# Kernel tuning notes

Measured on AMD Instinct MI355X. Metric: run time of the kernel, lower is better.

Reference implementation:

```python
import jax, jax.numpy as jnp
import numpy as np

C = 256          # C_in == C_out
G = C // 4       # groups = C_in/4 -> 4 channels per group
K = 3
STRIDE = 1
PAD = 2
DIL = 2
EPS = 1e-5

@jax.custom_vjp
def binarize(x):
    # 1-bit sign binarization with straight-through estimator (STE)
    return jnp.sign(x)

def _bin_fwd(x):
    return jnp.sign(x), x

def _bin_bwd(x, g):
    # STE with hardtanh clip: pass grad where |x| <= 1
    return (g * (jnp.abs(x) <= 1.0).astype(g.dtype),)

binarize.defvjp(_bin_fwd, _bin_bwd)

def setup_inputs() -> dict:
    key = jax.random.key(0)
    k1, k2, k3, k4, k5, k6 = jax.random.split(key, 6)
    x = jax.random.normal(k1, (64, C, 32, 32), jnp.float32)
    # grouped conv weight: [C_out, C_in/groups, K, K] = [256, 4, 3, 3]
    weight = jax.random.normal(k2, (C, C // G, K, K), jnp.float32) * 0.1
    gamma = 1.0 + 0.1 * jax.random.normal(k3, (C,), jnp.float32)
    beta = 0.1 * jax.random.normal(k4, (C,), jnp.float32)
    running_mean = 0.1 * jax.random.normal(k5, (C,), jnp.float32)
    running_var = jax.random.uniform(k6, (C,), jnp.float32, 0.5, 1.5)
    return {"x": x, "weight": weight, "gamma": gamma, "beta": beta,
            "running_mean": running_mean, "running_var": running_var}

def reference(x, weight, gamma, beta, running_mean, running_var):
    # BatchNorm2d (inference form with running stats)
    inv = gamma * jax.lax.rsqrt(running_var + EPS)            # [C]
    h = x * inv[None, :, None, None] + (beta - running_mean * inv)[None, :, None, None]
    # binarize activations and weights (1w1a)
    a = binarize(h)
    w = binarize(weight)
    # grouped dilated conv, stride 1, pad 2, dilation 2 -> same HxW
    out = jax.lax.conv_general_dilated(
        a, w,
        window_strides=(STRIDE, STRIDE),
        padding=[(PAD, PAD), (PAD, PAD)],
        rhs_dilation=(DIL, DIL),
        dimension_numbers=("NCHW", "OIHW", "NCHW"),
        feature_group_count=G)
    # channel shuffle: [N,C,H,W] -> [N,g,C/g,H,W] -> [N,C/g,g,H,W] -> [N,C,H,W]
    N, Cc, H, W = out.shape
    out = out.reshape(N, G, Cc // G, H, W).transpose(0, 2, 1, 3, 4).reshape(N, Cc, H, W)
    # identity shortcut (stride == 1)
    return out + x
```

## Files before the change

### kernel.cpp

```cpp
#include <hip/hip_runtime.h>

#ifndef __has_builtin
#define __has_builtin(x) 0
#endif

#if __has_builtin(__builtin_amdgcn_sdot4)
#define DOT4(a, b, c) __builtin_amdgcn_sdot4((a), (b), (c), false)
#else
__device__ __forceinline__ int dot4_sw(int a, int b, int c) {
#pragma unroll
    for (int k = 0; k < 4; ++k)
        c += (int)(signed char)((a >> (8 * k)) & 0xff) *
             (int)(signed char)((b >> (8 * k)) & 0xff);
    return c;
}
#define DOT4(a, b, c) dot4_sw((a), (b), (c))
#endif

constexpr int CH   = 256;
constexpr int NPIX = 1024;
constexpr float BN_EPS = 1e-5f;

__device__ __forceinline__ float rfl_f(float v) {
    return __int_as_float(__builtin_amdgcn_readfirstlane(__float_as_int(v)));
}

__global__ __launch_bounds__(256) void bconv(const float* __restrict__ x,
                                             const float* __restrict__ wgt,
                                             const float* __restrict__ gamma,
                                             const float* __restrict__ beta,
                                             const float* __restrict__ rmean,
                                             const float* __restrict__ rvar,
                                             float* __restrict__ out) {
    __shared__ int   wq_lds[36];
    __shared__ float bn_lds[8];

    const int tid  = threadIdx.x;
    const int n    = blockIdx.x >> 6;
    const int g    = blockIdx.x & 63;
    const int pix0 = tid * 4;
    const int row  = pix0 >> 5;
    const int col0 = pix0 & 31;
    const float* xn = x + n * CH * NPIX;
    float* on = out + n * CH * NPIX;

    float4 xv[3][4];
#pragma unroll
    for (int kh = 0; kh < 3; ++kh) {
        const int rs  = row + 2 * kh - 2;
        const int rsc = min(max(rs, 0), 31);
        const float* rp = xn + g * 4 * NPIX + rsc * 32 + col0;
#pragma unroll
        for (int ci = 0; ci < 4; ++ci)
            xv[kh][ci] = *(const float4*)(rp + ci * NPIX);
    }
    float4 sc[4];
#pragma unroll
    for (int c2 = 0; c2 < 4; ++c2)
        sc[c2] = *(const float4*)(xn + (c2 * 64 + g) * NPIX + pix0);

    if (tid < 144) {
        const int c2 = tid / 36, r = tid % 36, ci = r / 9, tap = r % 9;
        float w = wgt[g * 144 + tid];
        int s = (w > 0.f) ? 1 : ((w < 0.f) ? -1 : 0);
        ((char*)wq_lds)[(c2 * 9 + tap) * 4 + ci] = (char)s;
    } else if (tid < 148) {
        const int ci = tid - 144, c = g * 4 + ci;
        float r  = __fdiv_rn(1.0f, __fsqrt_rn(__fadd_rn(rvar[c], BN_EPS)));
        float iv = __fmul_rn(gamma[c], r);
        bn_lds[ci]     = iv;
        bn_lds[4 + ci] = __fsub_rn(beta[c], __fmul_rn(rmean[c], iv));
    }
    __syncthreads();

    int wq[4][9];
#pragma unroll
    for (int c2 = 0; c2 < 4; ++c2)
#pragma unroll
        for (int t = 0; t < 9; ++t)
            wq[c2][t] = __builtin_amdgcn_readfirstlane(wq_lds[c2 * 9 + t]);
    float inv[4], bias[4];
#pragma unroll
    for (int ci = 0; ci < 4; ++ci) {
        inv[ci]  = rfl_f(bn_lds[ci]);
        bias[ci] = rfl_f(bn_lds[4 + ci]);
    }

    int pkc[3][4];
#pragma unroll
    for (int kh = 0; kh < 3; ++kh) {
        const bool ok = (unsigned)(row + 2 * kh - 2) < 32u;
#pragma unroll
        for (int p = 0; p < 4; ++p) {
            int v = 0;
#pragma unroll
            for (int ci = 0; ci < 4; ++ci) {
                float h = __fadd_rn(__fmul_rn(((const float*)&xv[kh][ci])[p], inv[ci]), bias[ci]);
                int s = (h > 0.f) ? 1 : ((h < 0.f) ? -1 : 0);
                v |= (s & 0xff) << (8 * ci);
            }
            pkc[kh][p] = ok ? v : 0;
        }
    }

    const bool le = (col0 == 0), re = (col0 == 28);
    int a[3][8];
#pragma unroll
    for (int kh = 0; kh < 3; ++kh) {
        int l2 = __shfl_up(pkc[kh][2], 1);
        int l3 = __shfl_up(pkc[kh][3], 1);
        int r0 = __shfl_down(pkc[kh][0], 1);
        int r1 = __shfl_down(pkc[kh][1], 1);
        a[kh][0] = le ? 0 : l2;
        a[kh][1] = le ? 0 : l3;
        a[kh][2] = pkc[kh][0]; a[kh][3] = pkc[kh][1];
        a[kh][4] = pkc[kh][2]; a[kh][5] = pkc[kh][3];
        a[kh][6] = re ? 0 : r0;
        a[kh][7] = re ? 0 : r1;
    }

#pragma unroll
    for (int c2 = 0; c2 < 4; ++c2) {
        float4 o;
#pragma unroll
        for (int p = 0; p < 4; ++p) {
            int acc = 0;
#pragma unroll
            for (int kh = 0; kh < 3; ++kh)
#pragma unroll
                for (int kw = 0; kw < 3; ++kw)
                    acc = DOT4(a[kh][p + 2 * kw], wq[c2][kh * 3 + kw], acc);
            ((float*)&o)[p] = __fadd_rn((float)acc, ((const float*)&sc[c2])[p]);
        }
        *(float4*)(on + (c2 * 64 + g) * NPIX + pix0) = o;
    }
}

extern "C" void kernel_launch(void* const* d_in, const int* in_sizes, int n_in,
                              void* d_out, int out_size, void* d_ws, size_t ws_size,
                              hipStream_t stream) {
    const float* x     = (const float*)d_in[0];
    const float* wgt   = (const float*)d_in[1];
    const float* gamma = (const float*)d_in[2];
    const float* beta  = (const float*)d_in[3];
    const float* rmean = (const float*)d_in[4];
    const float* rvar  = (const float*)d_in[5];
    float* out = (float*)d_out;

    const int N = in_sizes[0] / (CH * NPIX);
    bconv<<<N * 64, 256, 0, stream>>>(x, wgt, gamma, beta, rmean, rvar, out);
}
```

Measured before the change: 34.59 us.

## Process two batch images per block and prefetch second image's input

Each block now handles two consecutive batch images for the same channel group, halving the grid size and amortizing the weight binarization and BN-parameter setup across both. The second image's input rows are loaded while the first image's packed activations are computed and stored, overlapping global loads with compute. A launch-bounds occupancy hint of four blocks is added. This raises register pressure and assumes an even batch size.

```diff
diff --git a/kernel.cpp b/kernel.cpp
--- a/kernel.cpp
+++ b/kernel.cpp
@@ -25,39 +25,46 @@
     return __int_as_float(__builtin_amdgcn_readfirstlane(__float_as_int(v)));
 }
 
-__global__ __launch_bounds__(256) void bconv(const float* __restrict__ x,
-                                             const float* __restrict__ wgt,
-                                             const float* __restrict__ gamma,
-                                             const float* __restrict__ beta,
-                                             const float* __restrict__ rmean,
-                                             const float* __restrict__ rvar,
-                                             float* __restrict__ out) {
+__global__ __launch_bounds__(256, 4)
+void bconv(const float* __restrict__ x,
+           const float* __restrict__ wgt,
+           const float* __restrict__ gamma,
+           const float* __restrict__ beta,
+           const float* __restrict__ rmean,
+           const float* __restrict__ rvar,
+           float* __restrict__ out) {
     __shared__ int   wq_lds[36];
     __shared__ float bn_lds[8];
 
     const int tid  = threadIdx.x;
-    const int n    = blockIdx.x >> 6;
+    const int n0   = (blockIdx.x >> 6) * 2;
     const int g    = blockIdx.x & 63;
     const int pix0 = tid * 4;
     const int row  = pix0 >> 5;
     const int col0 = pix0 & 31;
-    const float* xn = x + n * CH * NPIX;
-    float* on = out + n * CH * NPIX;
+    const float* xnA = x + n0 * CH * NPIX;
+    const float* xnB = xnA + CH * NPIX;
+    float* onA = out + n0 * CH * NPIX;
+    float* onB = onA + CH * NPIX;
 
     float4 xv[3][4];
+    auto load_xv = [&](const float* xn) {
 #pragma unroll
-    for (int kh = 0; kh < 3; ++kh) {
-        const int rs  = row + 2 * kh - 2;
-        const int rsc = min(max(rs, 0), 31);
-        const float* rp = xn + g * 4 * NPIX + rsc * 32 + col0;
+        for (int kh = 0; kh < 3; ++kh) {
+            const int rs  = row + 2 * kh - 2;
+            const int rsc = min(max(rs, 0), 31);
+            const float* rp = xn + g * 4 * NPIX + rsc * 32 + col0;
 #pragma unroll
-        for (int ci = 0; ci < 4; ++ci)
-            xv[kh][ci] = *(const float4*)(rp + ci * NPIX);
-    }
-    float4 sc[4];
+            for (int ci = 0; ci < 4; ++ci)
+                xv[kh][ci] = *(const float4*)(rp + ci * NPIX);
+        }
+    };
+
+    load_xv(xnA);
+    float4 scA[4];
 #pragma unroll
     for (int c2 = 0; c2 < 4; ++c2)
-        sc[c2] = *(const float4*)(xn + (c2 * 64 + g) * NPIX + pix0);
+        scA[c2] = *(const float4*)(xnA + (c2 * 64 + g) * NPIX + pix0);
 
     if (tid < 144) {
         const int c2 = tid / 36, r = tid % 36, ci = r / 9, tap = r % 9;
@@ -86,54 +93,73 @@
         bias[ci] = rfl_f(bn_lds[4 + ci]);
     }
 
-    int pkc[3][4];
+    auto pack = [&](int pkc[3][4]) {
 #pragma unroll
-    for (int kh = 0; kh < 3; ++kh) {
-        const bool ok = (unsigned)(row + 2 * kh - 2) < 32u;
+        for (int kh = 0; kh < 3; ++kh) {
+            const bool ok = (unsigned)(row + 2 * kh - 2) < 32u;
 #pragma unroll
-        for (int p = 0; p < 4; ++p) {
-            int v = 0;
+            for (int p = 0; p < 4; ++p) {
+                int v = 0;
 #pragma unroll
-            for (int ci = 0; ci < 4; ++ci) {
-                float h = __fadd_rn(__fmul_rn(((const float*)&xv[kh][ci])[p], inv[ci]), bias[ci]);
-                int s = (h > 0.f) ? 1 : ((h < 0.f) ? -1 : 0);
-                v |= (s & 0xff) << (8 * ci);
+                for (int ci = 0; ci < 4; ++ci) {
+                    float h = __fadd_rn(__fmul_rn(((const float*)&xv[kh][ci])[p], inv[ci]), bias[ci]);
+                    int s = (h > 0.f) ? 1 : ((h < 0.f) ? -1 : 0);
+                    v |= (s & 0xff) << (8 * ci);
+                }
+                pkc[kh][p] = ok ? v : 0;
             }
-            pkc[kh][p] = ok ? v : 0;
         }
-    }
+    };
 
     const bool le = (col0 == 0), re = (col0 == 28);
-    int a[3][8];
+    auto compute_store = [&](const int pkc[3][4], const float4 sc[4], float* on) {
+        int a[3][8];
 #pragma unroll
-    for (int kh = 0; kh < 3; ++kh) {
-        int l2 = __shfl_up(pkc[kh][2], 1);
-        int l3 = __shfl_up(pkc[kh][3], 1);
-        int r0 = __shfl_down(pkc[kh][0], 1);
-        int r1 = __shfl_down(pkc[kh][1], 1);
-        a[kh][0] = le ? 0 : l2;
-        a[kh][1] = le ? 0 : l3;
-        a[kh][2] = pkc[kh][0]; a[kh][3] = pkc[kh][1];
-        a[kh][4] = pkc[kh][2]; a[kh][5] = pkc[kh][3];
-        a[kh][6] = re ? 0 : r0;
-        a[kh][7] = re ? 0 : r1;
-    }
+        for (int kh = 0; kh < 3; ++kh) {
+            int l2 = __shfl_up(pkc[kh][2], 1);
+            int l3 = __shfl_up(pkc[kh][3], 1);
+            int r0 = __shfl_down(pkc[kh][0], 1);
+            int r1 = __shfl_down(pkc[kh][1], 1);
+            a[kh][0] = le ? 0 : l2;
+            a[kh][1] = le ? 0 : l3;
+            a[kh][2] = pkc[kh][0]; a[kh][3] = pkc[kh][1];
+            a[kh][4] = pkc[kh][2]; a[kh][5] = pkc[kh][3];
+            a[kh][6] = re ? 0 : r0;
+            a[kh][7] = re ? 0 : r1;
+        }
+#pragma unroll
+        for (int c2 = 0; c2 < 4; ++c2) {
+            float4 o;
+#pragma unroll
+            for (int p = 0; p < 4; ++p) {
+                int acc = 0;
+#pragma unroll
+                for (int kh = 0; kh < 3; ++kh)
+#pragma unroll
+                    for (int kw = 0; kw < 3; ++kw)
+                        acc = DOT4(a[kh][p + 2 * kw], wq[c2][kh * 3 + kw], acc);
+                ((float*)&o)[p] = __fadd_rn((float)acc, ((const float*)&sc[c2])[p]);
+            }
+            *(float4*)(on + (c2 * 64 + g) * NPIX + pix0) = o;
+        }
+    };
 
+    int pkcA[3][4];
+    pack(pkcA);
+
+    load_xv(xnB);
+
+    compute_store(pkcA, scA, onA);
+
+    int pkcB[3][4];
+    pack(pkcB);
+
+    float4 scB[4];
 #pragma unroll
-    for (int c2 = 0; c2 < 4; ++c2) {
-        float4 o;
-#pragma unroll
-        for (int p = 0; p < 4; ++p) {
-            int acc = 0;
-#pragma unroll
-            for (int kh = 0; kh < 3; ++kh)
-#pragma unroll
-                for (int kw = 0; kw < 3; ++kw)
-                    acc = DOT4(a[kh][p + 2 * kw], wq[c2][kh * 3 + kw], acc);
-            ((float*)&o)[p] = __fadd_rn((float)acc, ((const float*)&sc[c2])[p]);
-        }
-        *(float4*)(on + (c2 * 64 + g) * NPIX + pix0) = o;
-    }
+    for (int c2 = 0; c2 < 4; ++c2)
+        scB[c2] = *(const float4*)(xnB + (c2 * 64 + g) * NPIX + pix0);
+
+    compute_store(pkcB, scB, onB);
 }
 
 extern "C" void kernel_launch(void* const* d_in, const int* in_sizes, int n_in,
@@ -148,5 +174,5 @@
     float* out = (float*)d_out;
 
     const int N = in_sizes[0] / (CH * NPIX);
-    bconv<<<N * 64, 256, 0, stream>>>(x, wgt, gamma, beta, rmean, rvar, out);
+    bconv<<<(N / 2) * 64, 256, 0, stream>>>(x, wgt, gamma, beta, rmean, rvar, out);
 }
```

Result: faster. 33.77 us (-2.3%).
